# Optimization experiments

Hardware: AMD Instinct MI355X
Metric: run time of the kernel (lower is better)

The kernel has to match this reference:

```python
import jax, jax.numpy as jnp
import numpy as np

H = 36   # num_heads
D = 32   # head_dim
C = 1152 # hidden_size (== H*D)


def setup_inputs() -> dict:
    key = jax.random.key(0)
    k1, k2, k3, k4 = jax.random.split(key, 4)
    B, N = 4, 8192
    x = jax.random.normal(k1, (B, N, C), dtype=jnp.float32)
    # torch Linear(hidden, 3*inner, bias=False): we store as (in, out) for x @ W
    W_qkv = jax.random.normal(k2, (C, 3 * H * D), dtype=jnp.float32) * (1.0 / np.sqrt(C))
    W_out = jax.random.normal(k3, (H * D, C), dtype=jnp.float32) * (1.0 / np.sqrt(H * D))
    b_out = jax.random.normal(k4, (C,), dtype=jnp.float32) * 0.01
    return {"x": x, "W_qkv": W_qkv, "W_out": W_out, "b_out": b_out}


def reference(x, W_qkv, W_out, b_out):
    B, N, _ = x.shape
    qkv = (x @ W_qkv).reshape(B, N, 3, H, D)
    q = jax.nn.relu(qkv[:, :, 0])  # (B,N,H,D)
    k = jax.nn.relu(qkv[:, :, 1])
    v = qkv[:, :, 2]
    # kv state: per-head (D,D) outer-product sum over tokens
    kv = jnp.einsum('bnhd,bnhe->bhde', k, v)        # (B,H,D,D)
    out = jnp.einsum('bnhd,bhde->bnhe', q, kv)      # (B,N,H,D)
    k_sum = k.sum(axis=1)                            # (B,H,D)
    denom = jnp.einsum('bnhd,bhd->bnh', q, k_sum)[..., None] + 1e-6
    out = (out / denom).reshape(B, N, H * D)
    return out @ W_out + b_out
```

## Files before the change

kernel.cpp:

```cpp
#include <hip/hip_runtime.h>
#include <hip/hip_bf16.h>
#include <stdint.h>


#define HH 36
#define DD 32
#define CC 1152
#define NB 4
#define NN 8192
#define M_TOT (NB * NN)
#define N1 (3 * HH * DD)
#define HD (HH * DD)
#define HPB 3
#define KVSPLIT 32

typedef __attribute__((ext_vector_type(8))) short bf16x8;
typedef __attribute__((ext_vector_type(4))) float f32x4;

__device__ __forceinline__ uint16_t f2b(float f) {
  union { float f; uint32_t u; } v; v.f = f;
  uint32_t u = v.u;
  return (uint16_t)((u + 0x7fffu + ((u >> 16) & 1u)) >> 16);
}
__device__ __forceinline__ float uasf(uint32_t u) {
  union { uint32_t u; float f; } v; v.u = u; return v.f;
}
__device__ __forceinline__ void unpack8v(uint4 u, f32x4& lo, f32x4& hi) {
  lo[0] = uasf(u.x << 16); lo[1] = uasf(u.x & 0xffff0000u);
  lo[2] = uasf(u.y << 16); lo[3] = uasf(u.y & 0xffff0000u);
  hi[0] = uasf(u.z << 16); hi[1] = uasf(u.z & 0xffff0000u);
  hi[2] = uasf(u.w << 16); hi[3] = uasf(u.w & 0xffff0000u);
}

#define GLOAD16(g, l)                                                        \
  __builtin_amdgcn_global_load_lds(                                          \
      (const __attribute__((address_space(1))) void*)(g),                    \
      (__attribute__((address_space(3))) void*)(l), 16, 0, 0)

__global__ void zero_kernel(float* __restrict__ p, int n) {
  int i = blockIdx.x * blockDim.x + threadIdx.x;
  if (i < n) p[i] = 0.f;
}

__global__ void convert_kernel(const float* __restrict__ in, uint16_t* __restrict__ out, int n4) {
  int i = blockIdx.x * blockDim.x + threadIdx.x;
  if (i >= n4) return;
  float4 v = ((const float4*)in)[i];
  ushort4 o;
  o.x = f2b(v.x); o.y = f2b(v.y); o.z = f2b(v.z); o.w = f2b(v.w);
  ((ushort4*)out)[i] = o;
}

__global__ void transpose_convert_kernel(const float* __restrict__ in, uint16_t* __restrict__ out,
                                         int R, int Cc) {
  __shared__ uint16_t tile[32][33];
  int c0 = blockIdx.x * 32, r0 = blockIdx.y * 32;
  int tx = threadIdx.x & 31, ty = threadIdx.x >> 5;
#pragma unroll
  for (int i = 0; i < 4; i++) {
    int r = ty + i * 8;
    tile[r][tx] = f2b(in[(size_t)(r0 + r) * Cc + c0 + tx]);
  }
  __syncthreads();
#pragma unroll
  for (int i = 0; i < 4; i++) {
    int c = ty + i * 8;
    out[(size_t)(c0 + c) * R + r0 + tx] = tile[tx][c];
  }
}

template <int EPI, int NC>
__global__ __launch_bounds__(256, 4)
void gemm_bf16_kernel(const uint16_t* __restrict__ A, const uint16_t* __restrict__ BT,
                      uint16_t* __restrict__ outb, float* __restrict__ outf,
                      const float* __restrict__ bias, int K) {
  constexpr int NT = NC / 128;
  __shared__ uint16_t As[128 * 64];
  __shared__ uint16_t Bs[128 * 64];
  const int flat = blockIdx.y * NT + blockIdx.x;
  const int xcd = flat & 7;
  const int s = flat >> 3;
  const int n0 = (s % NT) * 128;
  const int m0 = ((s / NT) * 8 + xcd) * 128;
  const int t = threadIdx.x;
  const int lane = t & 63, w = t >> 6;
  const int wr = w >> 1, wc = w & 1;
  const int l15 = lane & 15, q4 = lane >> 4;
  f32x4 acc[4][4] = {};

  const int srow = w * 32 + (lane >> 3);
  const int sseg = ((lane & 7) ^ (lane >> 3)) * 8;
  const uint16_t* Ag = A + (size_t)(m0 + srow) * K + sseg;
  const uint16_t* Bg = BT + (size_t)(n0 + srow) * K + sseg;
  uint16_t* lA = &As[(w * 32) * 64];
  uint16_t* lB = &Bs[(w * 32) * 64];

  for (int k0 = 0; k0 < K; k0 += 64) {
    __syncthreads();
#pragma unroll
    for (int i = 0; i < 4; i++) {
      GLOAD16(Ag + k0 + (size_t)(i * 8) * K, lA + i * 8 * 64);
      GLOAD16(Bg + k0 + (size_t)(i * 8) * K, lB + i * 8 * 64);
    }
    __syncthreads();
#pragma unroll
    for (int kk = 0; kk < 2; kk++) {
      bf16x8 af[4], bfr[4];
      const int sbase = (kk * 4 + q4);
#pragma unroll
      for (int i = 0; i < 4; i++) {
        const int row = wr * 64 + i * 16 + l15;
        af[i] = *(const bf16x8*)&As[row * 64 + (sbase ^ (l15 & 7)) * 8];
      }
#pragma unroll
      for (int j = 0; j < 4; j++) {
        const int row = wc * 64 + j * 16 + l15;
        bfr[j] = *(const bf16x8*)&Bs[row * 64 + (sbase ^ (l15 & 7)) * 8];
      }
#pragma unroll
      for (int i = 0; i < 4; i++)
#pragma unroll
        for (int j = 0; j < 4; j++)
          acc[i][j] = __builtin_amdgcn_mfma_f32_16x16x32_bf16(af[i], bfr[j], acc[i][j], 0, 0, 0);
    }
  }
#pragma unroll
  for (int i = 0; i < 4; i++) {
#pragma unroll
    for (int j = 0; j < 4; j++) {
      int col = n0 + wc * 64 + j * 16 + l15;
#pragma unroll
      for (int r = 0; r < 4; r++) {
        int row = m0 + wr * 64 + i * 16 + q4 * 4 + r;
        float v = acc[i][j][r];
        if (EPI == 0) {
          if (col < 2 * HD) v = fmaxf(v, 0.f);
          outb[(size_t)row * NC + col] = f2b(v);
        } else {
          outf[(size_t)row * NC + col] = v + bias[col];
        }
      }
    }
  }
}

__global__ __launch_bounds__(64)
void kv_kernel(const uint16_t* __restrict__ qkvb, float* __restrict__ kvT, float* __restrict__ ksum) {
  __shared__ float kb[32][40];
  __shared__ float vb[32][40];
  const int bh = blockIdx.x / KVSPLIT;
  const int sp = blockIdx.x % KVSPLIT;
  const int b = bh / HH, h = bh % HH;
  const int t = threadIdx.x;
  const int d0 = (t >> 3) * 4, e0 = (t & 7) * 4;
  const int m0 = b * NN + sp * (NN / KVSPLIT);
  const size_t koff = (size_t)HD + h * DD;
  const size_t voff = (size_t)2 * HD + h * DD;
  float acc[4][4] = {};
  float ks[4] = {};
  const int srow = t >> 1, sseg = (t & 1) * 16;
  for (int c = 0; c < NN / KVSPLIT; c += 32) {
    const uint16_t* kp = qkvb + (size_t)(m0 + c + srow) * N1 + koff + sseg;
    const uint16_t* vp = qkvb + (size_t)(m0 + c + srow) * N1 + voff + sseg;
    uint4 kr0 = *(const uint4*)kp;
    uint4 kr1 = *(const uint4*)(kp + 8);
    uint4 vr0 = *(const uint4*)vp;
    uint4 vr1 = *(const uint4*)(vp + 8);
    f32x4 klo, khi, klo2, khi2, vlo, vhi, vlo2, vhi2;
    unpack8v(kr0, klo, khi); unpack8v(kr1, klo2, khi2);
    unpack8v(vr0, vlo, vhi); unpack8v(vr1, vlo2, vhi2);
    __syncthreads();
    *(f32x4*)&kb[srow][sseg + 0] = klo;  *(f32x4*)&kb[srow][sseg + 4] = khi;
    *(f32x4*)&kb[srow][sseg + 8] = klo2; *(f32x4*)&kb[srow][sseg + 12] = khi2;
    *(f32x4*)&vb[srow][sseg + 0] = vlo;  *(f32x4*)&vb[srow][sseg + 4] = vhi;
    *(f32x4*)&vb[srow][sseg + 8] = vlo2; *(f32x4*)&vb[srow][sseg + 12] = vhi2;
    __syncthreads();
#pragma unroll 8
    for (int n = 0; n < 32; n++) {
      f32x4 kd = *(const f32x4*)&kb[n][d0];
      f32x4 ve = *(const f32x4*)&vb[n][e0];
#pragma unroll
      for (int i = 0; i < 4; i++)
#pragma unroll
        for (int j = 0; j < 4; j++) acc[i][j] += kd[i] * ve[j];
      if ((t & 7) == 0) {
#pragma unroll
        for (int i = 0; i < 4; i++) ks[i] += kd[i];
      }
    }
  }
#pragma unroll
  for (int i = 0; i < 4; i++)
#pragma unroll
    for (int j = 0; j < 4; j++)
      atomicAdd(&kvT[(size_t)bh * 1024 + (e0 + j) * DD + d0 + i], acc[i][j]);
  if ((t & 7) == 0) {
#pragma unroll
    for (int i = 0; i < 4; i++) atomicAdd(&ksum[bh * DD + d0 + i], ks[i]);
  }
}

__global__ __launch_bounds__(256)
void attn_kernel(const uint16_t* __restrict__ qkvb, const float* __restrict__ kvT,
                 const float* __restrict__ ksum, uint16_t* __restrict__ attn) {
  const int t = threadIdx.x;
  const int lane = t & 63, w = t >> 6;
  const int mbase = blockIdx.x * 256 + w * 64;
  const int b = mbase >> 13;
  const int e = lane & 31, dh = lane >> 5;
  const int h0 = blockIdx.y * HPB;
  for (int hh = 0; hh < HPB; hh++) {
    const int h = h0 + hh;
    const int bh = b * HH + h;
    const float* kvp = kvT + (size_t)bh * 1024 + e * DD + dh * 16;
    f32x4 kva = *(const f32x4*)(kvp + 0);
    f32x4 kvb2 = *(const f32x4*)(kvp + 4);
    f32x4 kvc = *(const f32x4*)(kvp + 8);
    f32x4 kvd = *(const f32x4*)(kvp + 12);
    const float* ksp = ksum + bh * DD + dh * 16;
    f32x4 ksa = *(const f32x4*)(ksp + 0);
    f32x4 ksb = *(const f32x4*)(ksp + 4);
    f32x4 ksc = *(const f32x4*)(ksp + 8);
    f32x4 ksd = *(const f32x4*)(ksp + 12);
#pragma unroll 4
    for (int r = 0; r < 64; r++) {
      const int m = mbase + r;
      const uint16_t* qp = qkvb + (size_t)m * N1 + h * DD + dh * 16;
      uint4 q0 = *(const uint4*)qp;
      uint4 q1 = *(const uint4*)(qp + 8);
      f32x4 qa, qb2, qc, qd;
      unpack8v(q0, qa, qb2);
      unpack8v(q1, qc, qd);
      float o = 0.f, den = 0.f;
#pragma unroll
      for (int ii = 0; ii < 4; ii++) {
        o += qa[ii] * kva[ii];  den += qa[ii] * ksa[ii];
        o += qb2[ii] * kvb2[ii]; den += qb2[ii] * ksb[ii];
        o += qc[ii] * kvc[ii];  den += qc[ii] * ksc[ii];
        o += qd[ii] * kvd[ii];  den += qd[ii] * ksd[ii];
      }
      o += __shfl_xor(o, 32);
      den += __shfl_xor(den, 32);
      float res = o / (den + 1e-6f);
      if (dh == 0) attn[(size_t)m * HD + h * DD + e] = f2b(res);
    }
  }
}

extern "C" void kernel_launch(void* const* d_in, const int* in_sizes, int n_in,
                              void* d_out, int out_size, void* d_ws, size_t ws_size,
                              hipStream_t stream) {
  const float* x = (const float*)d_in[0];
  const float* Wqkv = (const float*)d_in[1];
  const float* Wout = (const float*)d_in[2];
  const float* bout = (const float*)d_in[3];
  float* y = (float*)d_out;
  char* ws = (char*)d_ws;
  uint16_t* xb = (uint16_t*)ws;
  uint16_t* wqkvT = (uint16_t*)(ws + 75497472);
  uint16_t* woutT = (uint16_t*)(ws + 83460096);
  uint16_t* qkvb = (uint16_t*)(ws + 86114304);
  float* kvT = (float*)(ws + 312606720);
  float* ksum = (float*)(ws + 313196544);
  uint16_t* attn = xb;

  zero_kernel<<<(152064 + 255) / 256, 256, 0, stream>>>(kvT, 152064);
  convert_kernel<<<(M_TOT * CC / 4) / 256, 256, 0, stream>>>(x, xb, M_TOT * CC / 4);
  transpose_convert_kernel<<<dim3(N1 / 32, CC / 32), 256, 0, stream>>>(Wqkv, wqkvT, CC, N1);
  transpose_convert_kernel<<<dim3(CC / 32, CC / 32), 256, 0, stream>>>(Wout, woutT, CC, CC);
  gemm_bf16_kernel<0, N1><<<dim3(N1 / 128, M_TOT / 128), 256, 0, stream>>>(xb, wqkvT, qkvb, nullptr, nullptr, CC);
  kv_kernel<<<144 * KVSPLIT, 64, 0, stream>>>(qkvb, kvT, ksum);
  attn_kernel<<<dim3(M_TOT / 256, HH / HPB), 256, 0, stream>>>(qkvb, kvT, ksum, attn);
  gemm_bf16_kernel<1, CC><<<dim3(CC / 128, M_TOT / 128), 256, 0, stream>>>(attn, woutT, nullptr, y, bout, CC);
}
```

Measured before the change: 962.8 us.

## Replace GEMMs with 256x256-tile double-buffered pipelined MFMA kernel

Both projection GEMMs move from a 128x128-tile, 4-wave kernel to a 256x256-tile, 8-wave kernel. K is fixed at 1152. The new kernel double-buffers LDS through a swizzled layout and interleaves global-to-LDS staging with four MFMA quadrants per K step, using explicit barriers, waitcnt and s_setprio. The aim is to hide load latency behind compute and raise reuse per LDS byte. N is not a multiple of 256, so partial tiles compute padded columns and read past the weight buffers into other workspace memory, with stores guarded. The Wout transpose now runs later so its buffer can reuse the qkv region.

```diff
diff --git a/kernel.cpp b/kernel.cpp
--- a/kernel.cpp
+++ b/kernel.cpp
@@ -1,5 +1,4 @@
 #include <hip/hip_runtime.h>
-#include <hip/hip_bf16.h>
 #include <stdint.h>
 
 
@@ -37,6 +36,17 @@
       (const __attribute__((address_space(1))) void*)(g),                    \
       (__attribute__((address_space(3))) void*)(l), 16, 0, 0)
 
+__device__ __forceinline__ int swz_off(int row, int col) {
+  int off = ((row >> 4) * 2 + (col >> 5)) * 1024 + (row & 15) * 64 + (col & 31) * 2;
+  return off ^ (((off >> 9) & 1) << 5);
+}
+__device__ __forceinline__ void stage_decode(int d, int& row, int& col) {
+  int lin = d ^ (((d >> 9) & 1) << 5);
+  int s = lin >> 10;
+  row = (s >> 1) * 16 + ((lin >> 6) & 15);
+  col = (s & 1) * 32 + ((lin >> 1) & 31);
+}
+
 __global__ void zero_kernel(float* __restrict__ p, int n) {
   int i = blockIdx.x * blockDim.x + threadIdx.x;
   if (i < n) p[i] = 0.f;
@@ -69,79 +79,170 @@
   }
 }
 
-template <int EPI, int NC>
-__global__ __launch_bounds__(256, 4)
-void gemm_bf16_kernel(const uint16_t* __restrict__ A, const uint16_t* __restrict__ BT,
-                      uint16_t* __restrict__ outb, float* __restrict__ outf,
-                      const float* __restrict__ bias, int K) {
-  constexpr int NT = NC / 128;
-  __shared__ uint16_t As[128 * 64];
-  __shared__ uint16_t Bs[128 * 64];
-  const int flat = blockIdx.y * NT + blockIdx.x;
-  const int xcd = flat & 7;
-  const int s = flat >> 3;
-  const int n0 = (s % NT) * 128;
-  const int m0 = ((s / NT) * 8 + xcd) * 128;
-  const int t = threadIdx.x;
-  const int lane = t & 63, w = t >> 6;
-  const int wr = w >> 1, wc = w & 1;
+template <int EPI, int NREAL>
+__global__ __launch_bounds__(512, 2)
+void gemm256_kernel(const uint16_t* __restrict__ A, const uint16_t* __restrict__ BT,
+                    uint16_t* __restrict__ outb, float* __restrict__ outf,
+                    const float* __restrict__ bias) {
+  constexpr int K = 1152;
+  constexpr int NTT = K / 64;
+  constexpr int NTx = (EPI == 0) ? 14 : 5;
+  __shared__ uint16_t lds[2][4][8192];
+
+  const int flat = blockIdx.y * NTx + blockIdx.x;
+  const int xcd = flat & 7, sg = flat >> 3;
+  const int n0 = (sg % NTx) * 256;
+  const int m0 = ((sg / NTx) * 8 + xcd) * 256;
+  const int tid = threadIdx.x;
+  const int lane = tid & 63, w = tid >> 6;
+  const int wm = w >> 2, wn = w & 3;
   const int l15 = lane & 15, q4 = lane >> 4;
-  f32x4 acc[4][4] = {};
-
-  const int srow = w * 32 + (lane >> 3);
-  const int sseg = ((lane & 7) ^ (lane >> 3)) * 8;
-  const uint16_t* Ag = A + (size_t)(m0 + srow) * K + sseg;
-  const uint16_t* Bg = BT + (size_t)(n0 + srow) * K + sseg;
-  uint16_t* lA = &As[(w * 32) * 64];
-  uint16_t* lB = &Bs[(w * 32) * 64];
-
-  for (int k0 = 0; k0 < K; k0 += 64) {
-    __syncthreads();
-#pragma unroll
-    for (int i = 0; i < 4; i++) {
-      GLOAD16(Ag + k0 + (size_t)(i * 8) * K, lA + i * 8 * 64);
-      GLOAD16(Bg + k0 + (size_t)(i * 8) * K, lB + i * 8 * 64);
-    }
-    __syncthreads();
-#pragma unroll
-    for (int kk = 0; kk < 2; kk++) {
-      bf16x8 af[4], bfr[4];
-      const int sbase = (kk * 4 + q4);
-#pragma unroll
-      for (int i = 0; i < 4; i++) {
-        const int row = wr * 64 + i * 16 + l15;
-        af[i] = *(const bf16x8*)&As[row * 64 + (sbase ^ (l15 & 7)) * 8];
-      }
-#pragma unroll
-      for (int j = 0; j < 4; j++) {
-        const int row = wc * 64 + j * 16 + l15;
-        bfr[j] = *(const bf16x8*)&Bs[row * 64 + (sbase ^ (l15 & 7)) * 8];
-      }
-#pragma unroll
-      for (int i = 0; i < 4; i++)
-#pragma unroll
-        for (int j = 0; j < 4; j++)
-          acc[i][j] = __builtin_amdgcn_mfma_f32_16x16x32_bf16(af[i], bfr[j], acc[i][j], 0, 0, 0);
-    }
-  }
-#pragma unroll
-  for (int i = 0; i < 4; i++) {
-#pragma unroll
-    for (int j = 0; j < 4; j++) {
-      int col = n0 + wc * 64 + j * 16 + l15;
-#pragma unroll
-      for (int r = 0; r < 4; r++) {
-        int row = m0 + wr * 64 + i * 16 + q4 * 4 + r;
-        float v = acc[i][j][r];
-        if (EPI == 0) {
-          if (col < 2 * HD) v = fmaxf(v, 0.f);
-          outb[(size_t)row * NC + col] = f2b(v);
-        } else {
-          outf[(size_t)row * NC + col] = v + bias[col];
+
+  int r0, c0, r1, c1;
+  stage_decode(tid * 16, r0, c0);
+  stage_decode(tid * 16 + 8192, r1, c1);
+  const size_t go0 = (size_t)r0 * K + c0;
+  const size_t go1 = (size_t)r1 * K + c1;
+  const uint16_t* A0p = A + (size_t)m0 * K;
+  const uint16_t* A1p = A + (size_t)(m0 + 128) * K;
+  const uint16_t* B0p = BT + (size_t)n0 * K;
+  const uint16_t* B1p = BT + (size_t)(n0 + 128) * K;
+  const int stl = w * 512;
+
+#define STAGE(bp, kt, slot)                                                  \
+  {                                                                          \
+    const uint16_t* _g = (bp) + (size_t)(kt) * 64;                           \
+    GLOAD16(_g + go0, (slot) + stl);                                         \
+    GLOAD16(_g + go1, (slot) + 4096 + stl);                                  \
+  }
+#define LGKM0()                                           \
+  asm volatile("s_waitcnt lgkmcnt(0)" ::: "memory");      \
+  __builtin_amdgcn_sched_barrier(0)
+
+  f32x4 acc[8][4] = {};
+  bf16x8 a[4][2], b[2][2][2];
+
+  STAGE(B1p, 0, &lds[0][3][0]);
+  STAGE(A1p, 0, &lds[0][1][0]);
+  STAGE(A0p, 0, &lds[0][0][0]);
+  STAGE(B0p, 0, &lds[0][2][0]);
+  STAGE(B1p, 1, &lds[1][3][0]);
+  STAGE(A1p, 1, &lds[1][1][0]);
+  asm volatile("s_waitcnt vmcnt(4)" ::: "memory");
+  __builtin_amdgcn_s_barrier();
+
+#pragma unroll 2
+  for (int T = 0; T < NTT; T++) {
+    const int cur = T & 1;
+    const int tn = (T + 1 < NTT) ? T + 1 : NTT - 1;
+    const int tn2 = (T + 2 < NTT) ? T + 2 : NTT - 1;
+    const uint16_t* sA = &lds[cur][wm][0];
+    const uint16_t* sB = &lds[cur][2 + (wn >> 1)][0];
+#pragma unroll
+    for (int i = 0; i < 4; i++)
+#pragma unroll
+      for (int kk = 0; kk < 2; kk++)
+        a[i][kk] = *(const bf16x8*)((const char*)sA +
+            swz_off(i * 16 + l15, kk * 32 + q4 * 8));
+#pragma unroll
+    for (int j = 0; j < 2; j++)
+#pragma unroll
+      for (int kk = 0; kk < 2; kk++)
+        b[0][j][kk] = *(const bf16x8*)((const char*)sB +
+            swz_off((wn & 1) * 64 + j * 16 + l15, kk * 32 + q4 * 8));
+    STAGE(A0p, tn, &lds[cur ^ 1][0][0]);
+    __builtin_amdgcn_s_barrier();
+    LGKM0();
+    __builtin_amdgcn_s_setprio(1);
+#pragma unroll
+    for (int i = 0; i < 4; i++)
+#pragma unroll
+      for (int j = 0; j < 2; j++)
+#pragma unroll
+        for (int kk = 0; kk < 2; kk++)
+          acc[i][j] = __builtin_amdgcn_mfma_f32_16x16x32_bf16(
+              a[i][kk], b[0][j][kk], acc[i][j], 0, 0, 0);
+    __builtin_amdgcn_s_setprio(0);
+    __builtin_amdgcn_s_barrier();
+#pragma unroll
+    for (int j = 0; j < 2; j++)
+#pragma unroll
+      for (int kk = 0; kk < 2; kk++)
+        b[1][j][kk] = *(const bf16x8*)((const char*)sB +
+            swz_off((wn & 1) * 64 + 32 + j * 16 + l15, kk * 32 + q4 * 8));
+    STAGE(B0p, tn, &lds[cur ^ 1][2][0]);
+    __builtin_amdgcn_s_barrier();
+    LGKM0();
+    __builtin_amdgcn_s_setprio(1);
+#pragma unroll
+    for (int i = 0; i < 4; i++)
+#pragma unroll
+      for (int j = 0; j < 2; j++)
+#pragma unroll
+        for (int kk = 0; kk < 2; kk++)
+          acc[i][2 + j] = __builtin_amdgcn_mfma_f32_16x16x32_bf16(
+              a[i][kk], b[1][j][kk], acc[i][2 + j], 0, 0, 0);
+    __builtin_amdgcn_s_setprio(0);
+    __builtin_amdgcn_s_barrier();
+#pragma unroll
+    for (int i = 0; i < 4; i++)
+#pragma unroll
+      for (int kk = 0; kk < 2; kk++)
+        a[i][kk] = *(const bf16x8*)((const char*)sA +
+            swz_off(64 + i * 16 + l15, kk * 32 + q4 * 8));
+    STAGE(B1p, tn2, &lds[cur][3][0]);
+    __builtin_amdgcn_s_barrier();
+    LGKM0();
+    __builtin_amdgcn_s_setprio(1);
+#pragma unroll
+    for (int i = 0; i < 4; i++)
+#pragma unroll
+      for (int j = 0; j < 2; j++)
+#pragma unroll
+        for (int kk = 0; kk < 2; kk++)
+          acc[4 + i][2 + j] = __builtin_amdgcn_mfma_f32_16x16x32_bf16(
+              a[i][kk], b[1][j][kk], acc[4 + i][2 + j], 0, 0, 0);
+    __builtin_amdgcn_s_setprio(0);
+    __builtin_amdgcn_s_barrier();
+    STAGE(A1p, tn2, &lds[cur][1][0]);
+    __builtin_amdgcn_s_barrier();
+    LGKM0();
+    __builtin_amdgcn_s_setprio(1);
+#pragma unroll
+    for (int i = 0; i < 4; i++)
+#pragma unroll
+      for (int j = 0; j < 2; j++)
+#pragma unroll
+        for (int kk = 0; kk < 2; kk++)
+          acc[4 + i][j] = __builtin_amdgcn_mfma_f32_16x16x32_bf16(
+              a[i][kk], b[0][j][kk], acc[4 + i][j], 0, 0, 0);
+    __builtin_amdgcn_s_setprio(0);
+    asm volatile("s_waitcnt vmcnt(4)" ::: "memory");
+    __builtin_amdgcn_s_barrier();
+  }
+  asm volatile("s_waitcnt vmcnt(0)" ::: "memory");
+#pragma unroll
+  for (int mi = 0; mi < 8; mi++) {
+    const int row = m0 + wm * 128 + mi * 16 + q4 * 4;
+#pragma unroll
+    for (int nj = 0; nj < 4; nj++) {
+      const int col = n0 + wn * 64 + nj * 16 + l15;
+      if (col < NREAL) {
+#pragma unroll
+        for (int r = 0; r < 4; r++) {
+          float v = acc[mi][nj][r];
+          if (EPI == 0) {
+            if (col < 2 * HD) v = fmaxf(v, 0.f);
+            outb[(size_t)(row + r) * NREAL + col] = f2b(v);
+          } else {
+            outf[(size_t)(row + r) * NREAL + col] = v + bias[col];
+          }
         }
       }
     }
   }
+#undef STAGE
+#undef LGKM0
 }
 
 __global__ __launch_bounds__(64)
@@ -258,18 +359,18 @@
   char* ws = (char*)d_ws;
   uint16_t* xb = (uint16_t*)ws;
   uint16_t* wqkvT = (uint16_t*)(ws + 75497472);
-  uint16_t* woutT = (uint16_t*)(ws + 83460096);
-  uint16_t* qkvb = (uint16_t*)(ws + 86114304);
-  float* kvT = (float*)(ws + 312606720);
-  float* ksum = (float*)(ws + 313196544);
+  uint16_t* qkvb = (uint16_t*)(ws + 83755008);
+  float* kvT = (float*)(ws + 310247424);
+  float* ksum = (float*)(ws + 310837248);
+  uint16_t* woutT = qkvb;
   uint16_t* attn = xb;
 
   zero_kernel<<<(152064 + 255) / 256, 256, 0, stream>>>(kvT, 152064);
   convert_kernel<<<(M_TOT * CC / 4) / 256, 256, 0, stream>>>(x, xb, M_TOT * CC / 4);
   transpose_convert_kernel<<<dim3(N1 / 32, CC / 32), 256, 0, stream>>>(Wqkv, wqkvT, CC, N1);
-  transpose_convert_kernel<<<dim3(CC / 32, CC / 32), 256, 0, stream>>>(Wout, woutT, CC, CC);
-  gemm_bf16_kernel<0, N1><<<dim3(N1 / 128, M_TOT / 128), 256, 0, stream>>>(xb, wqkvT, qkvb, nullptr, nullptr, CC);
+  gemm256_kernel<0, N1><<<dim3(14, 128), 512, 0, stream>>>(xb, wqkvT, qkvb, nullptr, nullptr);
   kv_kernel<<<144 * KVSPLIT, 64, 0, stream>>>(qkvb, kvT, ksum);
   attn_kernel<<<dim3(M_TOT / 256, HH / HPB), 256, 0, stream>>>(qkvb, kvT, ksum, attn);
-  gemm_bf16_kernel<1, CC><<<dim3(CC / 128, M_TOT / 128), 256, 0, stream>>>(attn, woutT, nullptr, y, bout, CC);
-}
+  transpose_convert_kernel<<<dim3(CC / 32, CC / 32), 256, 0, stream>>>(Wout, woutT, CC, CC);
+  gemm256_kernel<1, HD><<<dim3(5, 128), 512, 0, stream>>>(attn, woutT, nullptr, y, bout);
+}
```

New measurement: 987.1 us. +2.5%, slower.
